# Kernel tuning notes

Hardware: AMD Instinct MI355X
Metric: run time of the kernel (lower is better)

The kernel has to match this reference:

```python
import jax, jax.numpy as jnp
import numpy as np

N_STATE, N_CTRL, T, NB = 32, 16, 128, 64
NSC = N_STATE + N_CTRL

mT = lambda m: jnp.swapaxes(m, -1, -2)


def setup_inputs() -> dict:
    key = jax.random.key(0)
    k1, k2, k3, k4, k5, k6 = jax.random.split(key, 6)
    # Q must be PSD (the torch example builds Q = Qr^T Qr); add I for conditioning.
    Qr = jax.random.normal(k1, (NB, T, NSC, NSC), jnp.float32)
    Q = mT(Qr) @ Qr / NSC + jnp.eye(NSC, dtype=jnp.float32)
    p = jax.random.normal(k2, (NB, T, NSC), jnp.float32)
    x_init = jax.random.normal(k3, (NB, N_STATE), jnp.float32)
    # Stable-ish linear dynamics so the T=128 rollout does not blow up.
    A = jnp.tile(0.95 * jnp.eye(N_STATE, dtype=jnp.float32), (NB, 1, 1)) \
        + 0.02 * jax.random.normal(k4, (NB, N_STATE, N_STATE), jnp.float32)
    Bm = 0.1 * jax.random.normal(k5, (NB, N_STATE, N_CTRL), jnp.float32)
    c1 = 0.1 * jax.random.normal(k6, (NB, N_STATE), jnp.float32)
    return {"x_init": x_init, "Q": Q, "p": p, "A": A, "Bm": Bm, "c1": c1}


def _gains(Qt, qt, ns):
    # Qt: [B, nsc, nsc], qt: [B, nsc, 1]
    Qxx, Qxu = Qt[:, :ns, :ns], Qt[:, :ns, ns:]
    Qux, Quu = Qt[:, ns:, :ns], Qt[:, ns:, ns:]
    qx, qu = qt[:, :ns], qt[:, ns:]
    Quu_inv = jnp.linalg.pinv(Quu)          # batched pinv, as in the torch code
    K = -(Quu_inv @ Qux)                    # [B, nc, ns]
    k = -(Quu_inv @ qu)                     # [B, nc, 1]
    KT = mT(K)
    V = Qxx + Qxu @ K + KT @ Qux + KT @ Quu @ K
    v = qx + Qxu @ k + KT @ qu + KT @ Quu @ k
    return K, k, V, v


def _lqr(x_init, Q, p, A, Bm, c1):
    ns = A.shape[-1]
    F = jnp.concatenate([A, Bm], axis=-1)   # [B, ns, nsc]
    FT = mT(F)
    ft = c1[..., None]                       # [B, ns, 1]

    # ---- backward Riccati/DP recursion (sequential over T) ----
    K_last, k_last, V, v = _gains(Q[:, -1], p[:, -1][..., None], ns)

    def bstep(carry, inp):
        Vtp1, vtp1 = carry
        Qt_raw, pt = inp                     # [B,nsc,nsc], [B,nsc]
        Qt = Qt_raw + FT @ Vtp1 @ F
        qt = pt[..., None] + FT @ (Vtp1 @ ft) + FT @ vtp1
        K, k, Vt, vt = _gains(Qt, qt, ns)
        return (Vt, vt), (K, k)

    Qtm = jnp.swapaxes(Q[:, :-1], 0, 1)[::-1]   # [T-1, B, nsc, nsc], t = T-2..0
    ptm = jnp.swapaxes(p[:, :-1], 0, 1)[::-1]
    _, (Ks_rev, ks_rev) = jax.lax.scan(bstep, (V, v), (Qtm, ptm))
    Ks = jnp.concatenate([Ks_rev[::-1], K_last[None]], axis=0)  # [T, B, nc, ns], forward time order
    ks = jnp.concatenate([ks_rev[::-1], k_last[None]], axis=0)  # [T, B, nc, 1]

    # ---- forward rollout ----
    def fstep(x, inp):
        K, k, Qt, pt = inp
        u = jnp.einsum('bij,bj->bi', K, x) + k[..., 0]
        xu = jnp.concatenate([x, u], axis=-1)                 # tau_t, [B, nsc]
        obj = 0.5 * jnp.einsum('bi,bij,bj->b', xu, Qt, xu) + jnp.einsum('bi,bi->b', xu, pt)
        xn = jnp.einsum('bij,bj->bi', A, x) + jnp.einsum('bij,bj->bi', Bm, u) + c1
        return xn, (x, u, obj, xu)

    Qf = jnp.swapaxes(Q, 0, 1)               # [T, B, nsc, nsc]
    pf = jnp.swapaxes(p, 0, 1)
    _, (xs, us, objs, taus) = jax.lax.scan(fstep, x_init, (Ks, ks, Qf, pf))
    # xs: [T, B, ns] (x_0..x_{T-1}, matching torch which does not append x_T)
    return xs, us, objs, taus


def reference(x_init, Q, p, A, Bm, c1):
    return _lqr(x_init, Q, p, A, Bm, c1)
```

## Files before the change

### kernel.cpp

```cpp
#include <hip/hip_runtime.h>

#define TT     128
#define NBATCH 64

#define BAR()  asm volatile("s_waitcnt lgkmcnt(0)\n\ts_barrier" ::: "memory")
#define BARV() asm volatile("s_waitcnt vmcnt(0) lgkmcnt(0)\n\ts_barrier" ::: "memory")

__device__ __forceinline__ void gload16(const float* g, float* l) {
    __builtin_amdgcn_global_load_lds(
        (__attribute__((address_space(1))) void*)g,
        (__attribute__((address_space(3))) void*)l, 16, 0, 0);
}

__device__ __forceinline__ void inv4(const float4 pr[4], float IP[4][4]) {
    float a00=pr[0].x, a01=pr[0].y, a10=pr[1].x, a11=pr[1].y;
    float b00=pr[0].z, b01=pr[0].w, b10=pr[1].z, b11=pr[1].w;
    float c00=pr[2].x, c01=pr[2].y, c10=pr[3].x, c11=pr[3].y;
    float d00=pr[2].z, d01=pr[2].w, d10=pr[3].z, d11=pr[3].w;
    float r = 1.0f / (a00*a11 - a01*a10);
    float ia00 =  a11*r, ia01 = -a01*r, ia10 = -a10*r, ia11 = a00*r;
    float t00 = ia00*b00 + ia01*b10, t01 = ia00*b01 + ia01*b11;
    float t10 = ia10*b00 + ia11*b10, t11 = ia10*b01 + ia11*b11;
    float u00 = c00*ia00 + c01*ia10, u01 = c00*ia01 + c01*ia11;
    float u10 = c10*ia00 + c11*ia10, u11 = c10*ia01 + c11*ia11;
    float s00 = d00 - (c00*t00 + c01*t10), s01 = d01 - (c00*t01 + c01*t11);
    float s10 = d10 - (c10*t00 + c11*t10), s11 = d11 - (c10*t01 + c11*t11);
    float rs = 1.0f / (s00*s11 - s01*s10);
    float is00 =  s11*rs, is01 = -s01*rs, is10 = -s10*rs, is11 = s00*rs;
    float su00 = is00*u00 + is01*u10, su01 = is00*u01 + is01*u11;
    float su10 = is10*u00 + is11*u10, su11 = is10*u01 + is11*u11;
    IP[0][0] = ia00 + (t00*su00 + t01*su10);
    IP[0][1] = ia01 + (t00*su01 + t01*su11);
    IP[1][0] = ia10 + (t10*su00 + t11*su10);
    IP[1][1] = ia11 + (t10*su01 + t11*su11);
    IP[0][2] = -(t00*is00 + t01*is10);  IP[0][3] = -(t00*is01 + t01*is11);
    IP[1][2] = -(t10*is00 + t11*is10);  IP[1][3] = -(t10*is01 + t11*is11);
    IP[2][0] = -su00; IP[2][1] = -su01;
    IP[3][0] = -su10; IP[3][1] = -su11;
    IP[2][2] = is00;  IP[2][3] = is01;
    IP[3][2] = is10;  IP[3][3] = is11;
}

__global__ __launch_bounds__(256, 1)
void lqr_backward(const float* __restrict__ Q, const float* __restrict__ p,
                  const float* __restrict__ A, const float* __restrict__ Bm,
                  const float* __restrict__ c1, float* __restrict__ Kws)
{
    const int b   = blockIdx.x;
    const int tid = threadIdx.x;

    __shared__ __align__(16) float Fs[32*52];
    __shared__ __align__(16) float FTs[48*33];
    __shared__ __align__(16) float Vs[32*36];
    __shared__ __align__(16) float Ms[32*52];
    __shared__ __align__(16) float Qtb[2][48*48];
    __shared__ __align__(16) float qtb[2][256];
    __shared__ __align__(16) float Wa[16*52];
    __shared__ __align__(16) float Wb[16*52];
    __shared__ float vsv[32], fts[32], wv[32];

    for (int s = tid; s < 256; s += 256) {
        int k = s >> 3, q = s & 7;
        float4 v = ((const float4*)A)[(b*32 + k)*8 + q];
        ((float4*)(Fs + k*52))[q] = v;
        FTs[(4*q+0)*33 + k] = v.x; FTs[(4*q+1)*33 + k] = v.y;
        FTs[(4*q+2)*33 + k] = v.z; FTs[(4*q+3)*33 + k] = v.w;
    }
    for (int s = tid; s < 128; s += 256) {
        int k = s >> 2, q = s & 3;
        float4 v = ((const float4*)Bm)[(b*32 + k)*4 + q];
        ((float4*)(Fs + k*52))[8 + q] = v;
        FTs[(32+4*q+0)*33 + k] = v.x; FTs[(32+4*q+1)*33 + k] = v.y;
        FTs[(32+4*q+2)*33 + k] = v.z; FTs[(32+4*q+3)*33 + k] = v.w;
    }
    for (int s = tid; s < 288; s += 256) ((float4*)Vs)[s] = make_float4(0,0,0,0);
    if (tid < 32) { vsv[tid] = 0.0f; fts[tid] = c1[b*32 + tid]; }

    {
        const float* Qs0 = Q + (size_t)(b*TT + TT-1) * 2304;
        #pragma unroll
        for (int r = 0; r < 3; ++r) {
            int e = r*256 + tid;
            if (e < 576) gload16(Qs0 + e*4, Qtb[0] + e*4);
        }
        if (tid < 12) gload16(p + (size_t)(b*TT + TT-1)*48 + tid*4, qtb[0] + tid*4);
    }
    BARV();

    for (int t = TT-1; t >= 0; --t) {
        const int cur = (TT-1 - t) & 1;
        float* Qtc = Qtb[cur];
        float* qtc = qtb[cur];

        if (tid < 192) {
            const int i0 = (tid/12)*2, jq = tid%12;
            float4 a0 = make_float4(0,0,0,0), a1 = make_float4(0,0,0,0);
            #pragma unroll
            for (int k = 0; k < 32; ++k) {
                float v0 = Vs[k*36 + i0], v1 = Vs[k*36 + i0 + 1];
                float4 f = ((const float4*)(Fs + k*52))[jq];
                a0.x += v0*f.x; a0.y += v0*f.y; a0.z += v0*f.z; a0.w += v0*f.w;
                a1.x += v1*f.x; a1.y += v1*f.y; a1.z += v1*f.z; a1.w += v1*f.w;
            }
            ((float4*)(Ms + (i0  )*52))[jq] = a0;
            ((float4*)(Ms + (i0+1)*52))[jq] = a1;
        } else {
            const int idx = tid - 192;
            if (t > 0) {
                const float* Qs = Q + (size_t)(b*TT + t-1) * 2304;
                float* dst = Qtb[cur ^ 1];
                #pragma unroll
                for (int r = 0; r < 9; ++r) {
                    int e = r*64 + idx;
                    gload16(Qs + e*4, dst + e*4);
                }
                if (idx < 12) gload16(p + (size_t)(b*TT + t-1)*48 + idx*4,
                                      qtb[cur ^ 1] + idx*4);
            }
            if (idx < 32) {
                float acc = vsv[idx];
                #pragma unroll
                for (int k = 0; k < 32; ++k) acc += Vs[idx*36 + k] * fts[k];
                wv[idx] = acc;
            }
        }
        BAR();

        if (tid < 192) {
            const int r0 = (tid/12)*3, cq = tid%12;
            float4 a0 = ((float4*)Qtc)[(r0+0)*12 + cq];
            float4 a1 = ((float4*)Qtc)[(r0+1)*12 + cq];
            float4 a2 = ((float4*)Qtc)[(r0+2)*12 + cq];
            #pragma unroll
            for (int k = 0; k < 32; ++k) {
                float f0 = FTs[(r0+0)*33 + k];
                float f1 = FTs[(r0+1)*33 + k];
                float f2 = FTs[(r0+2)*33 + k];
                float4 m4 = ((const float4*)Ms)[k*13 + cq];
                a0.x += f0*m4.x; a0.y += f0*m4.y; a0.z += f0*m4.z; a0.w += f0*m4.w;
                a1.x += f1*m4.x; a1.y += f1*m4.y; a1.z += f1*m4.z; a1.w += f1*m4.w;
                a2.x += f2*m4.x; a2.y += f2*m4.y; a2.z += f2*m4.z; a2.w += f2*m4.w;
            }
            ((float4*)Qtc)[(r0+0)*12 + cq] = a0;
            ((float4*)Qtc)[(r0+1)*12 + cq] = a1;
            ((float4*)Qtc)[(r0+2)*12 + cq] = a2;
        } else if (tid < 240) {
            const int c = tid - 192;
            float acc = qtc[c];
            #pragma unroll
            for (int k = 0; k < 32; ++k) acc += FTs[c*33 + k] * wv[k];
            qtc[c] = acc;
        }
        BAR();

        float* Kbase = Kws + (size_t)(b*TT + t) * 528;
        #pragma unroll
        for (int q = 0; q < 4; ++q) {
            const float* S = (q == 0) ? nullptr : ((q & 1) ? Wa : Wb);
            float*       D = (q & 1) ? Wb : Wa;
            const int pc = 4*q;

            float4 pr[4];
            #pragma unroll
            for (int m = 0; m < 4; ++m) {
                if (q == 0) pr[m] = *(const float4*)(Qtc + (32 + m)*48 + 32);
                else        pr[m] = *(const float4*)(S + (4*q + m)*52 + 32 + pc);
            }
            float IP[4][4];
            inv4(pr, IP);

            if (tid < 196) {
                const int c  = tid >> 2;
                const int rg = tid & 3;
                float sn[4], R[4];
                #pragma unroll
                for (int n = 0; n < 4; ++n) {
                    int rr = 4*q + n;
                    sn[n] = (q == 0) ? ((c < 48) ? Qtc[(32+rr)*48 + c] : qtc[32 + rr])
                                     : S[rr*52 + c];
                }
                #pragma unroll
                for (int m = 0; m < 4; ++m)
                    R[m] = IP[m][0]*sn[0] + IP[m][1]*sn[1] + IP[m][2]*sn[2] + IP[m][3]*sn[3];

                #pragma unroll
                for (int i2 = 0; i2 < 4; ++i2) {
                    const int r = 4*rg + i2;
                    float val;
                    if (rg == q) {
                        val = R[i2];
                    } else {
                        float4 f;
                        if (q == 0) f = *(const float4*)(Qtc + (32 + r)*48 + 32);
                        else        f = *(const float4*)(S + r*52 + 32 + pc);
                        float src = (q == 0) ? ((c < 48) ? Qtc[(32+r)*48 + c] : qtc[32 + r])
                                             : S[r*52 + c];
                        val = src - (f.x*R[0] + f.y*R[1] + f.z*R[2] + f.w*R[3]);
                    }
                    D[r*52 + c] = val;
                    if (q == 3) {
                        if (c < 32)       Kbase[c*16 + r] = -val;
                        else if (c == 48) Kbase[512 + r]  = -val;
                    }
                }
            }
            BAR();
        }

        {
            const int i = tid >> 3, jq = tid & 7;
            float4 acc = ((float4*)Qtc)[i*12 + jq];
            float qx[16];
            #pragma unroll
            for (int kq = 0; kq < 4; ++kq) {
                float4 v4 = ((float4*)Qtc)[i*12 + 8 + kq];
                qx[kq*4+0] = v4.x; qx[kq*4+1] = v4.y;
                qx[kq*4+2] = v4.z; qx[kq*4+3] = v4.w;
            }
            #pragma unroll
            for (int k = 0; k < 16; ++k) {
                float4 kk = ((const float4*)Wb)[k*13 + jq];
                acc.x -= qx[k]*kk.x; acc.y -= qx[k]*kk.y;
                acc.z -= qx[k]*kk.z; acc.w -= qx[k]*kk.w;
            }
            ((float4*)Ms)[i*13 + jq] = acc;
        }
        BAR();

        if (tid < 32) {
            float acc = qtc[tid];
            #pragma unroll
            for (int k = 0; k < 16; ++k)
                acc -= Qtc[tid*48 + 32 + k] * Wb[k*52 + 48];
            vsv[tid] = acc;
        }
        #pragma unroll
        for (int rep = 0; rep < 4; ++rep) {
            int e = tid + rep*256;
            int i = e >> 5, j = e & 31;
            if (i <= j) {
                float sv = 0.5f * (Ms[i*52 + j] + Ms[j*52 + i]);
                Vs[i*36 + j] = sv; Vs[j*36 + i] = sv;
            }
        }
        BARV();
    }
}

__global__ __launch_bounds__(64, 1)
void lqr_forward(const float* __restrict__ Kws, const float* __restrict__ A,
                 const float* __restrict__ Bm, const float* __restrict__ c1,
                 const float* __restrict__ x_init,
                 float* __restrict__ xs, float* __restrict__ us,
                 float* __restrict__ taus)
{
    const int b = blockIdx.x, l = threadIdx.x;
    __shared__ __align__(16) float Fb[32*48];
    __shared__ __align__(16) float Kb[544];
    __shared__ float c1s[32], xu[48];

    for (int s = l; s < 256; s += 64) {
        int k = s >> 3, q = s & 7;
        ((float4*)Fb)[k*12 + q] = ((const float4*)A)[(b*32 + k)*8 + q];
    }
    for (int s = l; s < 128; s += 64) {
        int k = s >> 2, q = s & 3;
        ((float4*)Fb)[k*12 + 8 + q] = ((const float4*)Bm)[(b*32 + k)*4 + q];
    }
    if (l < 32) { c1s[l] = c1[b*32 + l]; xu[l] = x_init[b*32 + l]; }
    __syncthreads();

    for (int t = 0; t < TT; ++t) {
        const float4* src = (const float4*)(Kws + (size_t)(b*TT + t) * 528);
        ((float4*)Kb)[l]      = src[l];
        ((float4*)Kb)[l + 64] = src[l + 64];
        if (l < 4) ((float4*)Kb)[l + 128] = src[l + 128];
        __syncthreads();

        float part = 0.0f;
        int i = l & 15, g = l >> 4;
        #pragma unroll
        for (int jj = 0; jj < 8; ++jj) {
            int j = g*8 + jj;
            part += Kb[j*16 + i] * xu[j];
        }
        part += __shfl_down(part, 32);
        part += __shfl_down(part, 16);
        float ui = part + Kb[512 + i];
        if (l < 16) {
            xu[32 + l] = ui;
            us[(size_t)(t*64 + b)*16 + l] = ui;
        }
        __syncthreads();

        if (l < 32) xs[(size_t)(t*64 + b)*32 + l] = xu[l];
        if (l < 48) taus[(size_t)(t*64 + b)*48 + l] = xu[l];

        float pn = 0.0f;
        int i2 = l & 31, h = l >> 5;
        #pragma unroll
        for (int jj = 0; jj < 24; ++jj) {
            int j = h*24 + jj;
            pn += Fb[i2*48 + j] * xu[j];
        }
        pn += __shfl_down(pn, 32);
        float xni = pn + ((l < 32) ? c1s[i2] : 0.0f);
        __syncthreads();
        if (l < 32) xu[l] = xni;
        __syncthreads();
    }
}

__global__ __launch_bounds__(256, 4)
void lqr_obj(const float* __restrict__ Q, const float* __restrict__ p,
             const float* __restrict__ taus, float* __restrict__ objs)
{
    const int bi = blockIdx.x;
    const int b = bi >> 7, t = bi & 127;
    const int tid = threadIdx.x;
    __shared__ float xu[48];
    __shared__ float red[8];
    const float* tp = taus + (size_t)(t*64 + b)*48;
    if (tid < 48) xu[tid] = tp[tid];
    __syncthreads();

    const float4* Q4 = (const float4*)(Q + (size_t)bi * 2304);
    float acc = 0.0f;
    for (int e4 = tid; e4 < 576; e4 += 256) {
        float4 qv = Q4[e4];
        int r = e4 / 12, c = (e4 % 12) * 4;
        float xr = xu[r];
        acc += xr * (qv.x*xu[c] + qv.y*xu[c+1] + qv.z*xu[c+2] + qv.w*xu[c+3]);
    }
    acc *= 0.5f;
    if (tid < 48) acc += xu[tid] * p[(size_t)bi*48 + tid];

    #pragma unroll
    for (int off = 32; off > 0; off >>= 1) acc += __shfl_down(acc, off);
    if ((tid & 63) == 0) red[tid >> 6] = acc;
    __syncthreads();
    if (tid == 0) objs[(t << 6) + b] = red[0] + red[1] + red[2] + red[3];
}

extern "C" void kernel_launch(void* const* d_in, const int* in_sizes, int n_in,
                              void* d_out, int out_size, void* d_ws, size_t ws_size,
                              hipStream_t stream) {
    const float* x_init = (const float*)d_in[0];
    const float* Q      = (const float*)d_in[1];
    const float* p      = (const float*)d_in[2];
    const float* A      = (const float*)d_in[3];
    const float* Bm     = (const float*)d_in[4];
    const float* c1     = (const float*)d_in[5];

    float* out  = (float*)d_out;
    float* xs   = out;
    float* us   = out + 262144;
    float* objs = out + 393216;
    float* taus = out + 401408;

    float* Kws = (float*)d_ws;

    lqr_backward<<<NBATCH, 256, 0, stream>>>(Q, p, A, Bm, c1, Kws);
    lqr_forward<<<NBATCH, 64, 0, stream>>>(Kws, A, Bm, c1, x_init, xs, us, taus);
    lqr_obj<<<NBATCH*TT, 256, 0, stream>>>(Q, p, taus, objs);
}
```

Before: 838.2 us.

## Restructure Riccati matmuls with 4x4 register tiles and prefetch forward gains

New measurement: 780.6 us. 1.07x faster.

```diff
diff --git a/kernel.cpp b/kernel.cpp
--- a/kernel.cpp
+++ b/kernel.cpp
@@ -50,9 +50,9 @@
     const int tid = threadIdx.x;
 
     __shared__ __align__(16) float Fs[32*52];
-    __shared__ __align__(16) float FTs[48*33];
     __shared__ __align__(16) float Vs[32*36];
     __shared__ __align__(16) float Ms[32*52];
+    __shared__ __align__(16) float Xs[48*52];
     __shared__ __align__(16) float Qtb[2][48*48];
     __shared__ __align__(16) float qtb[2][256];
     __shared__ __align__(16) float Wa[16*52];
@@ -61,17 +61,11 @@
 
     for (int s = tid; s < 256; s += 256) {
         int k = s >> 3, q = s & 7;
-        float4 v = ((const float4*)A)[(b*32 + k)*8 + q];
-        ((float4*)(Fs + k*52))[q] = v;
-        FTs[(4*q+0)*33 + k] = v.x; FTs[(4*q+1)*33 + k] = v.y;
-        FTs[(4*q+2)*33 + k] = v.z; FTs[(4*q+3)*33 + k] = v.w;
+        ((float4*)(Fs + k*52))[q] = ((const float4*)A)[(b*32 + k)*8 + q];
     }
     for (int s = tid; s < 128; s += 256) {
         int k = s >> 2, q = s & 3;
-        float4 v = ((const float4*)Bm)[(b*32 + k)*4 + q];
-        ((float4*)(Fs + k*52))[8 + q] = v;
-        FTs[(32+4*q+0)*33 + k] = v.x; FTs[(32+4*q+1)*33 + k] = v.y;
-        FTs[(32+4*q+2)*33 + k] = v.z; FTs[(32+4*q+3)*33 + k] = v.w;
+        ((float4*)(Fs + k*52))[8 + q] = ((const float4*)Bm)[(b*32 + k)*4 + q];
     }
     for (int s = tid; s < 288; s += 256) ((float4*)Vs)[s] = make_float4(0,0,0,0);
     if (tid < 32) { vsv[tid] = 0.0f; fts[tid] = c1[b*32 + tid]; }
@@ -92,19 +86,23 @@
         float* Qtc = Qtb[cur];
         float* qtc = qtb[cur];
 
-        if (tid < 192) {
-            const int i0 = (tid/12)*2, jq = tid%12;
-            float4 a0 = make_float4(0,0,0,0), a1 = make_float4(0,0,0,0);
+        if (tid < 96) {
+            const int i0 = (tid/12)*4, c0 = (tid%12)*4;
+            float4 a0 = make_float4(0,0,0,0), a1 = a0, a2 = a0, a3 = a0;
             #pragma unroll
             for (int k = 0; k < 32; ++k) {
-                float v0 = Vs[k*36 + i0], v1 = Vs[k*36 + i0 + 1];
-                float4 f = ((const float4*)(Fs + k*52))[jq];
-                a0.x += v0*f.x; a0.y += v0*f.y; a0.z += v0*f.z; a0.w += v0*f.w;
-                a1.x += v1*f.x; a1.y += v1*f.y; a1.z += v1*f.z; a1.w += v1*f.w;
-            }
-            ((float4*)(Ms + (i0  )*52))[jq] = a0;
-            ((float4*)(Ms + (i0+1)*52))[jq] = a1;
-        } else {
+                float4 v = *(const float4*)(Vs + k*36 + i0);
+                float4 f = *(const float4*)(Fs + k*52 + c0);
+                a0.x += v.x*f.x; a0.y += v.x*f.y; a0.z += v.x*f.z; a0.w += v.x*f.w;
+                a1.x += v.y*f.x; a1.y += v.y*f.y; a1.z += v.y*f.z; a1.w += v.y*f.w;
+                a2.x += v.z*f.x; a2.y += v.z*f.y; a2.z += v.z*f.z; a2.w += v.z*f.w;
+                a3.x += v.w*f.x; a3.y += v.w*f.y; a3.z += v.w*f.z; a3.w += v.w*f.w;
+            }
+            *(float4*)(Ms + (i0+0)*52 + c0) = a0;
+            *(float4*)(Ms + (i0+1)*52 + c0) = a1;
+            *(float4*)(Ms + (i0+2)*52 + c0) = a2;
+            *(float4*)(Ms + (i0+3)*52 + c0) = a3;
+        } else if (tid >= 192) {
             const int idx = tid - 192;
             if (t > 0) {
                 const float* Qs = Q + (size_t)(b*TT + t-1) * 2304;
@@ -126,46 +124,46 @@
         }
         BAR();
 
-        if (tid < 192) {
-            const int r0 = (tid/12)*3, cq = tid%12;
-            float4 a0 = ((float4*)Qtc)[(r0+0)*12 + cq];
-            float4 a1 = ((float4*)Qtc)[(r0+1)*12 + cq];
-            float4 a2 = ((float4*)Qtc)[(r0+2)*12 + cq];
+        if (tid < 144) {
+            const int r0 = (tid/12)*4, c0 = (tid%12)*4;
+            float4 a0 = *(const float4*)(Qtc + (r0+0)*48 + c0);
+            float4 a1 = *(const float4*)(Qtc + (r0+1)*48 + c0);
+            float4 a2 = *(const float4*)(Qtc + (r0+2)*48 + c0);
+            float4 a3 = *(const float4*)(Qtc + (r0+3)*48 + c0);
             #pragma unroll
             for (int k = 0; k < 32; ++k) {
-                float f0 = FTs[(r0+0)*33 + k];
-                float f1 = FTs[(r0+1)*33 + k];
-                float f2 = FTs[(r0+2)*33 + k];
-                float4 m4 = ((const float4*)Ms)[k*13 + cq];
-                a0.x += f0*m4.x; a0.y += f0*m4.y; a0.z += f0*m4.z; a0.w += f0*m4.w;
-                a1.x += f1*m4.x; a1.y += f1*m4.y; a1.z += f1*m4.z; a1.w += f1*m4.w;
-                a2.x += f2*m4.x; a2.y += f2*m4.y; a2.z += f2*m4.z; a2.w += f2*m4.w;
-            }
-            ((float4*)Qtc)[(r0+0)*12 + cq] = a0;
-            ((float4*)Qtc)[(r0+1)*12 + cq] = a1;
-            ((float4*)Qtc)[(r0+2)*12 + cq] = a2;
-        } else if (tid < 240) {
+                float4 fr = *(const float4*)(Fs + k*52 + r0);
+                float4 mc = *(const float4*)(Ms + k*52 + c0);
+                a0.x += fr.x*mc.x; a0.y += fr.x*mc.y; a0.z += fr.x*mc.z; a0.w += fr.x*mc.w;
+                a1.x += fr.y*mc.x; a1.y += fr.y*mc.y; a1.z += fr.y*mc.z; a1.w += fr.y*mc.w;
+                a2.x += fr.z*mc.x; a2.y += fr.z*mc.y; a2.z += fr.z*mc.z; a2.w += fr.z*mc.w;
+                a3.x += fr.w*mc.x; a3.y += fr.w*mc.y; a3.z += fr.w*mc.z; a3.w += fr.w*mc.w;
+            }
+            *(float4*)(Xs + (r0+0)*52 + c0) = a0;
+            *(float4*)(Xs + (r0+1)*52 + c0) = a1;
+            *(float4*)(Xs + (r0+2)*52 + c0) = a2;
+            *(float4*)(Xs + (r0+3)*52 + c0) = a3;
+        } else if (tid >= 192 && tid < 240) {
             const int c = tid - 192;
             float acc = qtc[c];
             #pragma unroll
-            for (int k = 0; k < 32; ++k) acc += FTs[c*33 + k] * wv[k];
+            for (int k = 0; k < 32; ++k) acc += Fs[k*52 + c] * wv[k];
             qtc[c] = acc;
+            if (c >= 32) Xs[c*52 + 48] = acc;
         }
         BAR();
 
         float* Kbase = Kws + (size_t)(b*TT + t) * 528;
         #pragma unroll
         for (int q = 0; q < 4; ++q) {
-            const float* S = (q == 0) ? nullptr : ((q & 1) ? Wa : Wb);
+            const float* S = (q == 0) ? (Xs + 32*52) : ((q & 1) ? Wa : Wb);
             float*       D = (q & 1) ? Wb : Wa;
             const int pc = 4*q;
 
             float4 pr[4];
             #pragma unroll
-            for (int m = 0; m < 4; ++m) {
-                if (q == 0) pr[m] = *(const float4*)(Qtc + (32 + m)*48 + 32);
-                else        pr[m] = *(const float4*)(S + (4*q + m)*52 + 32 + pc);
-            }
+            for (int m = 0; m < 4; ++m)
+                pr[m] = *(const float4*)(S + (4*q + m)*52 + 32 + pc);
             float IP[4][4];
             inv4(pr, IP);
 
@@ -174,11 +172,7 @@
                 const int rg = tid & 3;
                 float sn[4], R[4];
                 #pragma unroll
-                for (int n = 0; n < 4; ++n) {
-                    int rr = 4*q + n;
-                    sn[n] = (q == 0) ? ((c < 48) ? Qtc[(32+rr)*48 + c] : qtc[32 + rr])
-                                     : S[rr*52 + c];
-                }
+                for (int n = 0; n < 4; ++n) sn[n] = S[(4*q + n)*52 + c];
                 #pragma unroll
                 for (int m = 0; m < 4; ++m)
                     R[m] = IP[m][0]*sn[0] + IP[m][1]*sn[1] + IP[m][2]*sn[2] + IP[m][3]*sn[3];
@@ -190,11 +184,8 @@
                     if (rg == q) {
                         val = R[i2];
                     } else {
-                        float4 f;
-                        if (q == 0) f = *(const float4*)(Qtc + (32 + r)*48 + 32);
-                        else        f = *(const float4*)(S + r*52 + 32 + pc);
-                        float src = (q == 0) ? ((c < 48) ? Qtc[(32+r)*48 + c] : qtc[32 + r])
-                                             : S[r*52 + c];
+                        float4 f = *(const float4*)(S + r*52 + 32 + pc);
+                        float src = S[r*52 + c];
                         val = src - (f.x*R[0] + f.y*R[1] + f.z*R[2] + f.w*R[3]);
                     }
                     D[r*52 + c] = val;
@@ -208,39 +199,28 @@
         }
 
         {
-            const int i = tid >> 3, jq = tid & 7;
-            float4 acc = ((float4*)Qtc)[i*12 + jq];
-            float qx[16];
-            #pragma unroll
-            for (int kq = 0; kq < 4; ++kq) {
-                float4 v4 = ((float4*)Qtc)[i*12 + 8 + kq];
-                qx[kq*4+0] = v4.x; qx[kq*4+1] = v4.y;
-                qx[kq*4+2] = v4.z; qx[kq*4+3] = v4.w;
+            const int i = tid >> 3, j0 = (tid & 7) * 4;
+            float4 acc = *(const float4*)(Xs + i*52 + j0);
+            float qxu[16];
+            #pragma unroll
+            for (int m = 0; m < 4; ++m) {
+                float4 v4 = *(const float4*)(Xs + i*52 + 32 + m*4);
+                qxu[m*4+0] = v4.x; qxu[m*4+1] = v4.y;
+                qxu[m*4+2] = v4.z; qxu[m*4+3] = v4.w;
             }
             #pragma unroll
             for (int k = 0; k < 16; ++k) {
-                float4 kk = ((const float4*)Wb)[k*13 + jq];
-                acc.x -= qx[k]*kk.x; acc.y -= qx[k]*kk.y;
-                acc.z -= qx[k]*kk.z; acc.w -= qx[k]*kk.w;
-            }
-            ((float4*)Ms)[i*13 + jq] = acc;
-        }
-        BAR();
-
-        if (tid < 32) {
-            float acc = qtc[tid];
-            #pragma unroll
-            for (int k = 0; k < 16; ++k)
-                acc -= Qtc[tid*48 + 32 + k] * Wb[k*52 + 48];
-            vsv[tid] = acc;
-        }
-        #pragma unroll
-        for (int rep = 0; rep < 4; ++rep) {
-            int e = tid + rep*256;
-            int i = e >> 5, j = e & 31;
-            if (i <= j) {
-                float sv = 0.5f * (Ms[i*52 + j] + Ms[j*52 + i]);
-                Vs[i*36 + j] = sv; Vs[j*36 + i] = sv;
+                float4 kk = *(const float4*)(Wb + k*52 + j0);
+                acc.x -= qxu[k]*kk.x; acc.y -= qxu[k]*kk.y;
+                acc.z -= qxu[k]*kk.z; acc.w -= qxu[k]*kk.w;
+            }
+            *(float4*)(Vs + i*36 + j0) = acc;
+            if ((tid & 7) == 0) {
+                float accv = qtc[i];
+                #pragma unroll
+                for (int k = 0; k < 16; ++k)
+                    accv -= qxu[k] * Wb[k*52 + 48];
+                vsv[i] = accv;
             }
         }
         BARV();
@@ -268,14 +248,26 @@
         ((float4*)Fb)[k*12 + 8 + q] = ((const float4*)Bm)[(b*32 + k)*4 + q];
     }
     if (l < 32) { c1s[l] = c1[b*32 + l]; xu[l] = x_init[b*32 + l]; }
+
+    float4 ka, kb, kc = make_float4(0,0,0,0);
+    {
+        const float4* s0 = (const float4*)(Kws + (size_t)(b*TT) * 528);
+        ka = s0[l]; kb = s0[l + 64];
+        if (l < 4) kc = s0[l + 128];
+    }
     __syncthreads();
 
     for (int t = 0; t < TT; ++t) {
-        const float4* src = (const float4*)(Kws + (size_t)(b*TT + t) * 528);
-        ((float4*)Kb)[l]      = src[l];
-        ((float4*)Kb)[l + 64] = src[l + 64];
-        if (l < 4) ((float4*)Kb)[l + 128] = src[l + 128];
+        ((float4*)Kb)[l]      = ka;
+        ((float4*)Kb)[l + 64] = kb;
+        if (l < 4) ((float4*)Kb)[l + 128] = kc;
         __syncthreads();
+
+        if (t + 1 < TT) {
+            const float4* sn = (const float4*)(Kws + (size_t)(b*TT + t+1) * 528);
+            ka = sn[l]; kb = sn[l + 64];
+            if (l < 4) kc = sn[l + 128];
+        }
 
         float part = 0.0f;
         int i = l & 15, g = l >> 4;
```
